# Kernel tuning notes

Hardware: AMD Instinct MI355X
Metric: run time of the kernel (lower is better)

The kernel has to match this reference:

```python
import jax, jax.numpy as jnp
import numpy as np

FS = 3        # filter_size
STRIDE = 2
UPPER_PAD = 1
D_MODEL = 512


def setup_inputs() -> dict:
    key = jax.random.key(0)
    k1, k2, k3, k4 = jax.random.split(key, 4)
    b, h, n, d = 4, 8, 2048, D_MODEL
    nc = n // STRIDE
    layer_query = jax.random.normal(k1, (b, h, n, d), dtype=jnp.float32)
    uncompress_in = jax.random.normal(k2, (b, h, nc, d), dtype=jnp.float32)
    # nn.Linear(d*FS, d): weight (d, d*FS), bias (d,)
    W = jax.random.normal(k3, (d, d * FS), dtype=jnp.float32) * 0.02
    bias = jax.random.normal(k4, (d,), dtype=jnp.float32) * 0.01
    return {"layer_query": layer_query, "uncompress_in": uncompress_in,
            "W": W, "bias": bias, "i": 0}


def reference(layer_query, uncompress_in, W, bias, i):
    b, h, n, d = layer_query.shape
    # einsum('ijac,b->ijcab', u, kron_kernel) with kernel=[1,0,...] followed by
    # flatten(-2,-1) == transpose to (b,h,d,nc) then zero-upsample by STRIDE.
    u = jnp.swapaxes(uncompress_in, -1, -2)                      # (b,h,d,nc)
    nc = u.shape[-1]
    t = jnp.zeros(u.shape + (STRIDE,), u.dtype).at[..., 0].set(u)
    t = t.reshape(b, h, d, nc * STRIDE)                          # (b,h,d,nc*S)
    pad = FS - UPPER_PAD - 1
    t = jnp.pad(t, ((0, 0), (0, 0), (0, 0), (pad, pad)))
    # unfold(-1, FS, 1) then keep first n windows: window w covers t[..., w:w+FS]
    windows = jnp.stack([t[..., k:k + n] for k in range(FS)], axis=-1)  # (b,h,d,n,FS)
    up = jnp.transpose(windows, (0, 1, 3, 4, 2))                 # (b,h,n,FS,d)
    res_connect = up.sum(axis=3) / FS                            # (b,h,n,d)
    flat = up.reshape(b, h, n, FS * d)                           # (b,h,n,FS*d)
    out = jax.nn.relu(jnp.einsum('bhnk,dk->bhnd', flat, W) + bias)
    # dropout p=0.0 -> identity
    return layer_query + out + res_connect
```

## Files before the change

### kernel.cpp

```cpp
#include <hip/hip_runtime.h>
#include <cstdint>

#define NC    1024
#define D     512
#define KTOT  512
#define MTOT  32768
#define BK    32
#define NKC   16
#define ABYTES (129 * 64)
#define BBYTES (192 * 64)
#define BUFB   (ABYTES + BBYTES)

typedef short  short8  __attribute__((ext_vector_type(8)));
typedef float  floatx4 __attribute__((ext_vector_type(4)));

__device__ inline void gl2lds16(const void* gptr, void* lptr) {
  __builtin_amdgcn_global_load_lds(
      (const __attribute__((address_space(1))) void*)gptr,
      (__attribute__((address_space(3))) void*)lptr,
      16, 0, 0);
}

__device__ inline unsigned short f2bf_rne(float f) {
  union { float f; unsigned u; } x; x.f = f;
  unsigned r = x.u + 0x7fffu + ((x.u >> 16) & 1u);
  return (unsigned short)(r >> 16);
}

__global__ __launch_bounds__(256) void cvt_f32_bf16_all(
    const float* __restrict__ srcU, unsigned short* __restrict__ dstU, int n4U,
    const float* __restrict__ srcW, unsigned short* __restrict__ dstW, int n4W) {
  int i = blockIdx.x * 256 + threadIdx.x;
  const float* src;
  unsigned short* dst;
  int idx;
  if (i < n4U) {
    src = srcU; dst = dstU; idx = i;
  } else {
    idx = i - n4U;
    if (idx >= n4W) return;
    src = srcW; dst = dstW;
  }
  float4 v = ((const float4*)src)[idx];
  ushort4 o;
  o.x = f2bf_rne(v.x); o.y = f2bf_rne(v.y);
  o.z = f2bf_rne(v.z); o.w = f2bf_rne(v.w);
  ((ushort4*)dst)[idx] = o;
}

__global__ __launch_bounds__(256, 2) void fused_uncompress_gemm(
    const unsigned short* __restrict__ Ub,
    const unsigned short* __restrict__ Wb,
    const float* __restrict__ U32,
    const float* __restrict__ LQ,
    const float* __restrict__ bias,
    float* __restrict__ out)
{
  __shared__ __attribute__((aligned(16))) unsigned char smem[2 * BUFB];

  const int bid   = blockIdx.x;
  const int tileM = ((bid >> 6) << 3) | (bid & 7);
  const int tileN = (bid >> 3) & 7;
  const int r0 = tileM * 128;
  const int n0 = tileN * 64;
  const int tid  = threadIdx.x;
  const int wv   = tid >> 6;
  const int ln   = tid & 63;
  const int quad = ln >> 4;
  const int am   = ln & 15;

  floatx4 acc[2][12];
  #pragma unroll
  for (int rt = 0; rt < 2; ++rt)
    #pragma unroll
    for (int ct = 0; ct < 12; ++ct)
      acc[rt][ct] = floatx4{0.f, 0.f, 0.f, 0.f};

  const bool zeroExtra = (((r0 + 128) & (NC - 1)) == 0);

  auto stage = [&](int buf, int kc) {
    unsigned char* sA = smem + buf * BUFB;
    unsigned char* sB = sA + ABYTES;
    const int k0 = kc * BK;
    #pragma unroll
    for (int i = 0; i < 2; ++i) {
      int row = wv * 32 + i * 16 + (ln >> 2);
      int kch = (ln & 3) ^ (row & 3);
      const unsigned short* g = Ub + (size_t)(r0 + row) * KTOT + k0 + kch * 8;
      gl2lds16(g, sA + (wv * 32 + i * 16) * 64);
    }
    if (!zeroExtra && wv == 0 && ln < 4) {
      const unsigned short* g = Ub + (size_t)(r0 + 128) * KTOT + k0 + ln * 8;
      gl2lds16(g, sA + 128 * 64);
    }
    #pragma unroll
    for (int i = 0; i < 3; ++i) {
      int rho = wv * 48 + i * 16 + (ln >> 2);
      int kch = (ln & 3) ^ (rho & 3);
      int beta = rho >> 6;
      int nl   = rho & 63;
      const unsigned short* g =
          Wb + (size_t)(n0 + nl) * 1536 + beta * 512 + k0 + kch * 8;
      gl2lds16(g, sB + (wv * 48 + i * 16) * 64);
    }
  };

  if (zeroExtra && wv == 0 && ln < 4) {
    *(float4*)(smem + ABYTES - 64 + ln * 16)        = make_float4(0.f, 0.f, 0.f, 0.f);
    *(float4*)(smem + BUFB + ABYTES - 64 + ln * 16) = make_float4(0.f, 0.f, 0.f, 0.f);
  }
  stage(0, 0);
  __syncthreads();

  #pragma unroll 2
  for (int kc = 0; kc < NKC; ++kc) {
    const int cur = kc & 1;
    if (kc < NKC - 1) stage(cur ^ 1, kc + 1);

    unsigned char* sA = smem + cur * BUFB;
    unsigned char* sB = sA + ABYTES;
    short8 a0[2], a1[2];
    #pragma unroll
    for (int rt = 0; rt < 2; ++rt) {
      int row  = wv * 32 + rt * 16 + am;
      int sl   = quad ^ (row & 3);
      a0[rt] = *(const short8*)(sA + row * 64 + sl * 16);
      int row1 = row + 1;
      int sl1  = quad ^ (row1 & 3);
      a1[rt] = *(const short8*)(sA + row1 * 64 + sl1 * 16);
    }
    #pragma unroll
    for (int ct = 0; ct < 12; ++ct) {
      int beta = ct >> 2;
      int nl   = (ct & 3) * 16 + am;
      int rho  = beta * 64 + nl;
      int sl   = quad ^ (rho & 3);
      short8 b = *(const short8*)(sB + rho * 64 + sl * 16);
      #pragma unroll
      for (int rt = 0; rt < 2; ++rt) {
        acc[rt][ct] = __builtin_amdgcn_mfma_f32_16x16x32_bf16(
            (beta == 2) ? a1[rt] : a0[rt], b, acc[rt][ct], 0, 0, 0);
      }
    }
    __syncthreads();
  }

  const float inv3 = 1.0f / 3.0f;
  float* Ew = (float*)smem + (size_t)wv * 2 * 16 * 68;
  float* Ow = Ew + 16 * 68;

  #pragma unroll
  for (int rt = 0; rt < 2; ++rt) {
    #pragma unroll
    for (int dt = 0; dt < 4; ++dt) {
      float bv = bias[n0 + dt * 16 + am];
      #pragma unroll
      for (int r = 0; r < 4; ++r) {
        int row16 = quad * 4 + r;
        float p0 = acc[rt][dt][r];
        float p1 = acc[rt][4 + dt][r];
        float p2 = acc[rt][8 + dt][r];
        Ew[row16 * 68 + dt * 16 + am] = fmaxf(p1 + bv, 0.f);
        Ow[row16 * 68 + dt * 16 + am] = fmaxf(p0 + p2 + bv, 0.f);
      }
    }
    #pragma unroll
    for (int rr = 0; rr < 4; ++rr) {
      int row16 = rr * 4 + quad;
      int jl = wv * 32 + rt * 16 + row16;
      int j  = r0 + jl;
      int head = j >> 10;
      int jn   = j & (NC - 1);
      float4 ev = *(const float4*)(Ew + row16 * 68 + am * 4);
      float4 ov = *(const float4*)(Ow + row16 * 68 + am * 4);
      size_t ucol = (size_t)j * D + n0 + am * 4;
      float4 u0 = *(const float4*)(U32 + ucol);
      float4 u1 = make_float4(0.f, 0.f, 0.f, 0.f);
      if (jn != NC - 1) u1 = *(const float4*)(U32 + ucol + D);
      size_t ob = ((size_t)head * 2048 + 2 * jn) * D + n0 + am * 4;
      float4 lq0 = *(const float4*)(LQ + ob);
      float4 lq1 = *(const float4*)(LQ + ob + D);
      float4 o0, o1;
      o0.x = lq0.x + ev.x + u0.x * inv3;
      o0.y = lq0.y + ev.y + u0.y * inv3;
      o0.z = lq0.z + ev.z + u0.z * inv3;
      o0.w = lq0.w + ev.w + u0.w * inv3;
      o1.x = lq1.x + ov.x + (u0.x + u1.x) * inv3;
      o1.y = lq1.y + ov.y + (u0.y + u1.y) * inv3;
      o1.z = lq1.z + ov.z + (u0.z + u1.z) * inv3;
      o1.w = lq1.w + ov.w + (u0.w + u1.w) * inv3;
      *(float4*)(out + ob)     = o0;
      *(float4*)(out + ob + D) = o1;
    }
  }
}

extern "C" void kernel_launch(void* const* d_in, const int* in_sizes, int n_in,
                              void* d_out, int out_size, void* d_ws, size_t ws_size,
                              hipStream_t stream) {
  const float* LQ   = (const float*)d_in[0];
  const float* U32  = (const float*)d_in[1];
  const float* W    = (const float*)d_in[2];
  const float* bias = (const float*)d_in[3];
  float* out = (float*)d_out;

  unsigned short* Ub = (unsigned short*)d_ws;
  unsigned short* Wb = (unsigned short*)((char*)d_ws + (size_t)MTOT * KTOT * 2);

  const int n4U = MTOT * KTOT / 4;
  const int n4W = 512 * 1536 / 4;
  cvt_f32_bf16_all<<<(n4U + n4W + 255) / 256, 256, 0, stream>>>(
      U32, Ub, n4U, W, Wb, n4W);

  fused_uncompress_gemm<<<dim3(2048), dim3(256), 0, stream>>>(
      Ub, Wb, U32, LQ, bias, out);
}
```

Measured before the change: 321.0 us.

## Single-buffer LDS and split epilogue to raise occupancy to four blocks

Measured after the change: 410.5 us. 1.28x slower.

```diff
diff --git a/kernel.cpp b/kernel.cpp
--- a/kernel.cpp
+++ b/kernel.cpp
@@ -48,7 +48,7 @@
   ((ushort4*)dst)[idx] = o;
 }
 
-__global__ __launch_bounds__(256, 2) void fused_uncompress_gemm(
+__global__ __launch_bounds__(256, 4) void fused_uncompress_gemm(
     const unsigned short* __restrict__ Ub,
     const unsigned short* __restrict__ Wb,
     const float* __restrict__ U32,
@@ -56,7 +56,9 @@
     const float* __restrict__ bias,
     float* __restrict__ out)
 {
-  __shared__ __attribute__((aligned(16))) unsigned char smem[2 * BUFB];
+  __shared__ __attribute__((aligned(16))) unsigned char smem[BUFB];
+  unsigned char* smemA = smem;
+  unsigned char* smemB = smem + ABYTES;
 
   const int bid   = blockIdx.x;
   const int tileM = ((bid >> 6) << 3) | (bid & 7);
@@ -78,64 +80,52 @@
 
   const bool zeroExtra = (((r0 + 128) & (NC - 1)) == 0);
 
-  auto stage = [&](int buf, int kc) {
-    unsigned char* sA = smem + buf * BUFB;
-    unsigned char* sB = sA + ABYTES;
+  if (zeroExtra && wv == 0 && ln < 4)
+    *(float4*)(smemA + 128 * 64 + ln * 16) = make_float4(0.f, 0.f, 0.f, 0.f);
+
+  for (int kc = 0; kc < NKC; ++kc) {
     const int k0 = kc * BK;
+
     #pragma unroll
     for (int i = 0; i < 2; ++i) {
       int row = wv * 32 + i * 16 + (ln >> 2);
-      int kch = (ln & 3) ^ (row & 3);
+      int kch = (ln & 3) ^ ((row >> 1) & 3);
       const unsigned short* g = Ub + (size_t)(r0 + row) * KTOT + k0 + kch * 8;
-      gl2lds16(g, sA + (wv * 32 + i * 16) * 64);
+      gl2lds16(g, smemA + (wv * 32 + i * 16) * 64);
     }
     if (!zeroExtra && wv == 0 && ln < 4) {
       const unsigned short* g = Ub + (size_t)(r0 + 128) * KTOT + k0 + ln * 8;
-      gl2lds16(g, sA + 128 * 64);
+      gl2lds16(g, smemA + 128 * 64);
     }
     #pragma unroll
     for (int i = 0; i < 3; ++i) {
       int rho = wv * 48 + i * 16 + (ln >> 2);
-      int kch = (ln & 3) ^ (rho & 3);
+      int kch = (ln & 3) ^ ((rho >> 1) & 3);
       int beta = rho >> 6;
       int nl   = rho & 63;
       const unsigned short* g =
           Wb + (size_t)(n0 + nl) * 1536 + beta * 512 + k0 + kch * 8;
-      gl2lds16(g, sB + (wv * 48 + i * 16) * 64);
-    }
-  };
-
-  if (zeroExtra && wv == 0 && ln < 4) {
-    *(float4*)(smem + ABYTES - 64 + ln * 16)        = make_float4(0.f, 0.f, 0.f, 0.f);
-    *(float4*)(smem + BUFB + ABYTES - 64 + ln * 16) = make_float4(0.f, 0.f, 0.f, 0.f);
-  }
-  stage(0, 0);
-  __syncthreads();
-
-  #pragma unroll 2
-  for (int kc = 0; kc < NKC; ++kc) {
-    const int cur = kc & 1;
-    if (kc < NKC - 1) stage(cur ^ 1, kc + 1);
-
-    unsigned char* sA = smem + cur * BUFB;
-    unsigned char* sB = sA + ABYTES;
+      gl2lds16(g, smemB + (wv * 48 + i * 16) * 64);
+    }
+    __syncthreads();
+
     short8 a0[2], a1[2];
     #pragma unroll
     for (int rt = 0; rt < 2; ++rt) {
       int row  = wv * 32 + rt * 16 + am;
-      int sl   = quad ^ (row & 3);
-      a0[rt] = *(const short8*)(sA + row * 64 + sl * 16);
+      int sl   = quad ^ ((row >> 1) & 3);
+      a0[rt] = *(const short8*)(smemA + row * 64 + sl * 16);
       int row1 = row + 1;
-      int sl1  = quad ^ (row1 & 3);
-      a1[rt] = *(const short8*)(sA + row1 * 64 + sl1 * 16);
+      int sl1  = quad ^ ((row1 >> 1) & 3);
+      a1[rt] = *(const short8*)(smemA + row1 * 64 + sl1 * 16);
     }
     #pragma unroll
     for (int ct = 0; ct < 12; ++ct) {
       int beta = ct >> 2;
       int nl   = (ct & 3) * 16 + am;
       int rho  = beta * 64 + nl;
-      int sl   = quad ^ (rho & 3);
-      short8 b = *(const short8*)(sB + rho * 64 + sl * 16);
+      int sl   = quad ^ ((rho >> 1) & 3);
+      short8 b = *(const short8*)(smemB + rho * 64 + sl * 16);
       #pragma unroll
       for (int rt = 0; rt < 2; ++rt) {
         acc[rt][ct] = __builtin_amdgcn_mfma_f32_16x16x32_bf16(
@@ -146,50 +136,60 @@
   }
 
   const float inv3 = 1.0f / 3.0f;
-  float* Ew = (float*)smem + (size_t)wv * 2 * 16 * 68;
-  float* Ow = Ew + 16 * 68;
+  float* Sw = (float*)smem + (size_t)wv * 16 * 68;
+  float bv[4];
+  #pragma unroll
+  for (int dt = 0; dt < 4; ++dt) bv[dt] = bias[n0 + dt * 16 + am];
 
   #pragma unroll
   for (int rt = 0; rt < 2; ++rt) {
     #pragma unroll
-    for (int dt = 0; dt < 4; ++dt) {
-      float bv = bias[n0 + dt * 16 + am];
+    for (int dt = 0; dt < 4; ++dt)
       #pragma unroll
-      for (int r = 0; r < 4; ++r) {
-        int row16 = quad * 4 + r;
-        float p0 = acc[rt][dt][r];
-        float p1 = acc[rt][4 + dt][r];
-        float p2 = acc[rt][8 + dt][r];
-        Ew[row16 * 68 + dt * 16 + am] = fmaxf(p1 + bv, 0.f);
-        Ow[row16 * 68 + dt * 16 + am] = fmaxf(p0 + p2 + bv, 0.f);
-      }
-    }
+      for (int r = 0; r < 4; ++r)
+        Sw[(quad * 4 + r) * 68 + dt * 16 + am] =
+            fmaxf(acc[rt][4 + dt][r] + bv[dt], 0.f);
     #pragma unroll
     for (int rr = 0; rr < 4; ++rr) {
       int row16 = rr * 4 + quad;
-      int jl = wv * 32 + rt * 16 + row16;
-      int j  = r0 + jl;
+      int j  = r0 + wv * 32 + rt * 16 + row16;
       int head = j >> 10;
       int jn   = j & (NC - 1);
-      float4 ev = *(const float4*)(Ew + row16 * 68 + am * 4);
-      float4 ov = *(const float4*)(Ow + row16 * 68 + am * 4);
+      float4 ev = *(const float4*)(Sw + row16 * 68 + am * 4);
+      float4 u0 = *(const float4*)(U32 + (size_t)j * D + n0 + am * 4);
+      size_t ob = ((size_t)head * 2048 + 2 * jn) * D + n0 + am * 4;
+      float4 lq0 = *(const float4*)(LQ + ob);
+      float4 o0;
+      o0.x = lq0.x + ev.x + u0.x * inv3;
+      o0.y = lq0.y + ev.y + u0.y * inv3;
+      o0.z = lq0.z + ev.z + u0.z * inv3;
+      o0.w = lq0.w + ev.w + u0.w * inv3;
+      *(float4*)(out + ob) = o0;
+    }
+    #pragma unroll
+    for (int dt = 0; dt < 4; ++dt)
+      #pragma unroll
+      for (int r = 0; r < 4; ++r)
+        Sw[(quad * 4 + r) * 68 + dt * 16 + am] =
+            fmaxf(acc[rt][dt][r] + acc[rt][8 + dt][r] + bv[dt], 0.f);
+    #pragma unroll
+    for (int rr = 0; rr < 4; ++rr) {
+      int row16 = rr * 4 + quad;
+      int j  = r0 + wv * 32 + rt * 16 + row16;
+      int head = j >> 10;
+      int jn   = j & (NC - 1);
+      float4 ov = *(const float4*)(Sw + row16 * 68 + am * 4);
       size_t ucol = (size_t)j * D + n0 + am * 4;
       float4 u0 = *(const float4*)(U32 + ucol);
       float4 u1 = make_float4(0.f, 0.f, 0.f, 0.f);
       if (jn != NC - 1) u1 = *(const float4*)(U32 + ucol + D);
       size_t ob = ((size_t)head * 2048 + 2 * jn) * D + n0 + am * 4;
-      float4 lq0 = *(const float4*)(LQ + ob);
       float4 lq1 = *(const float4*)(LQ + ob + D);
-      float4 o0, o1;
-      o0.x = lq0.x + ev.x + u0.x * inv3;
-      o0.y = lq0.y + ev.y + u0.y * inv3;
-      o0.z = lq0.z + ev.z + u0.z * inv3;
-      o0.w = lq0.w + ev.w + u0.w * inv3;
+      float4 o1;
       o1.x = lq1.x + ov.x + (u0.x + u1.x) * inv3;
       o1.y = lq1.y + ov.y + (u0.y + u1.y) * inv3;
       o1.z = lq1.z + ov.z + (u0.z + u1.z) * inv3;
       o1.w = lq1.w + ov.w + (u0.w + u1.w) * inv3;
-      *(float4*)(out + ob)     = o0;
       *(float4*)(out + ob + D) = o1;
     }
   }
```

## Replace syncthreads with explicit vmcnt waits, change LDS swizzle, raise occupancy

Applied to the files above, without the earlier changes.

New measurement: 321.7 us. Within noise of the previous version (+0.2%).

```diff
diff --git a/kernel.cpp b/kernel.cpp
--- a/kernel.cpp
+++ b/kernel.cpp
@@ -48,7 +48,7 @@
   ((ushort4*)dst)[idx] = o;
 }
 
-__global__ __launch_bounds__(256, 2) void fused_uncompress_gemm(
+__global__ __launch_bounds__(256, 3) void fused_uncompress_gemm(
     const unsigned short* __restrict__ Ub,
     const unsigned short* __restrict__ Wb,
     const float* __restrict__ U32,
@@ -85,7 +85,7 @@
     #pragma unroll
     for (int i = 0; i < 2; ++i) {
       int row = wv * 32 + i * 16 + (ln >> 2);
-      int kch = (ln & 3) ^ (row & 3);
+      int kch = (ln & 3) ^ ((row >> 1) & 3);
       const unsigned short* g = Ub + (size_t)(r0 + row) * KTOT + k0 + kch * 8;
       gl2lds16(g, sA + (wv * 32 + i * 16) * 64);
     }
@@ -96,7 +96,7 @@
     #pragma unroll
     for (int i = 0; i < 3; ++i) {
       int rho = wv * 48 + i * 16 + (ln >> 2);
-      int kch = (ln & 3) ^ (rho & 3);
+      int kch = (ln & 3) ^ ((rho >> 1) & 3);
       int beta = rho >> 6;
       int nl   = rho & 63;
       const unsigned short* g =
@@ -110,12 +110,20 @@
     *(float4*)(smem + BUFB + ABYTES - 64 + ln * 16) = make_float4(0.f, 0.f, 0.f, 0.f);
   }
   stage(0, 0);
-  __syncthreads();
 
   #pragma unroll 2
   for (int kc = 0; kc < NKC; ++kc) {
     const int cur = kc & 1;
-    if (kc < NKC - 1) stage(cur ^ 1, kc + 1);
+    if (kc < NKC - 1) {
+      stage(cur ^ 1, kc + 1);
+      __builtin_amdgcn_sched_barrier(0);
+      asm volatile("s_waitcnt vmcnt(5) lgkmcnt(0)" ::: "memory");
+    } else {
+      __builtin_amdgcn_sched_barrier(0);
+      asm volatile("s_waitcnt vmcnt(0) lgkmcnt(0)" ::: "memory");
+    }
+    __builtin_amdgcn_s_barrier();
+    __builtin_amdgcn_sched_barrier(0);
 
     unsigned char* sA = smem + cur * BUFB;
     unsigned char* sB = sA + ABYTES;
@@ -123,10 +131,10 @@
     #pragma unroll
     for (int rt = 0; rt < 2; ++rt) {
       int row  = wv * 32 + rt * 16 + am;
-      int sl   = quad ^ (row & 3);
+      int sl   = quad ^ ((row >> 1) & 3);
       a0[rt] = *(const short8*)(sA + row * 64 + sl * 16);
       int row1 = row + 1;
-      int sl1  = quad ^ (row1 & 3);
+      int sl1  = quad ^ ((row1 >> 1) & 3);
       a1[rt] = *(const short8*)(sA + row1 * 64 + sl1 * 16);
     }
     #pragma unroll
@@ -134,7 +142,7 @@
       int beta = ct >> 2;
       int nl   = (ct & 3) * 16 + am;
       int rho  = beta * 64 + nl;
-      int sl   = quad ^ (rho & 3);
+      int sl   = quad ^ ((rho >> 1) & 3);
       short8 b = *(const short8*)(sB + rho * 64 + sl * 16);
       #pragma unroll
       for (int rt = 0; rt < 2; ++rt) {
@@ -142,33 +150,35 @@
             (beta == 2) ? a1[rt] : a0[rt], b, acc[rt][ct], 0, 0, 0);
       }
     }
-    __syncthreads();
+    __builtin_amdgcn_sched_barrier(0);
+    asm volatile("" ::: "memory");
+    __builtin_amdgcn_s_barrier();
+    __builtin_amdgcn_sched_barrier(0);
   }
 
   const float inv3 = 1.0f / 3.0f;
   float* Ew = (float*)smem + (size_t)wv * 2 * 16 * 68;
   float* Ow = Ew + 16 * 68;
+  float bv[4];
+  #pragma unroll
+  for (int dt = 0; dt < 4; ++dt) bv[dt] = bias[n0 + dt * 16 + am];
 
   #pragma unroll
   for (int rt = 0; rt < 2; ++rt) {
     #pragma unroll
     for (int dt = 0; dt < 4; ++dt) {
-      float bv = bias[n0 + dt * 16 + am];
       #pragma unroll
       for (int r = 0; r < 4; ++r) {
         int row16 = quad * 4 + r;
-        float p0 = acc[rt][dt][r];
-        float p1 = acc[rt][4 + dt][r];
-        float p2 = acc[rt][8 + dt][r];
-        Ew[row16 * 68 + dt * 16 + am] = fmaxf(p1 + bv, 0.f);
-        Ow[row16 * 68 + dt * 16 + am] = fmaxf(p0 + p2 + bv, 0.f);
+        Ew[row16 * 68 + dt * 16 + am] = fmaxf(acc[rt][4 + dt][r] + bv[dt], 0.f);
+        Ow[row16 * 68 + dt * 16 + am] =
+            fmaxf(acc[rt][dt][r] + acc[rt][8 + dt][r] + bv[dt], 0.f);
       }
     }
     #pragma unroll
     for (int rr = 0; rr < 4; ++rr) {
       int row16 = rr * 4 + quad;
-      int jl = wv * 32 + rt * 16 + row16;
-      int j  = r0 + jl;
+      int j  = r0 + wv * 32 + rt * 16 + row16;
       int head = j >> 10;
       int jn   = j & (NC - 1);
       float4 ev = *(const float4*)(Ew + row16 * 68 + am * 4);
```
